# Performance work log

Hardware: AMD Instinct MI355X
Metric: run time of the kernel (lower is better)

The kernel has to match this reference:

```python
import jax, jax.numpy as jnp
import numpy as np

N_SPOT = 30000
N_USER = 30000
E = 600000
SPLIT = 5
ATT_IN = 512
HEADS = 4
PER = ATT_IN // HEADS  # 128
HID = 256
N_LAYERS = 3


def _glorot(key, shape):
    fan_in, fan_out = shape[-2], shape[-1]
    lim = (6.0 / (fan_in + fan_out)) ** 0.5
    return jax.random.uniform(key, shape, jnp.float32, -lim, lim)


def setup_inputs() -> dict:
    key = jax.random.key(0)
    ks = jax.random.split(key, 16)
    return {
        "x_spot": jax.random.normal(ks[0], (N_SPOT, SPLIT * ATT_IN), jnp.float32),
        "x_user": jax.random.normal(ks[1], (N_USER, 512), jnp.float32),
        "edge_us": jax.random.randint(ks[2], (2, E), 0, N_USER),  # user -> spot
        "edge_su": jax.random.randint(ks[3], (2, E), 0, N_SPOT),  # spot -> user
        "W_att": _glorot(ks[4], (HEADS, ATT_IN, PER)),
        "q_att": 1.414 * _glorot(ks[5], (HEADS, PER, 1)),
        "W0_us": _glorot(ks[6], (512, HID)),   # layer0 source weight, user->spot
        "W0_su": _glorot(ks[7], (512, HID)),   # layer0 source weight, spot->user
        "Wmid_us": _glorot(ks[8], (N_LAYERS - 1, HID, HID)),
        "Wmid_su": _glorot(ks[9], (N_LAYERS - 1, HID, HID)),
        "W_out_spot": _glorot(ks[10], (HID, 1)),
        "b_out_spot": jnp.zeros((1,), jnp.float32),
        "W_out_user": _glorot(ks[11], (HID, 1)),
        "b_out_user": jnp.zeros((1,), jnp.float32),
    }


def _edge_div(edge, n_src, n_dst):
    # sqrt(deg_src[e_src] * deg_dst[e_dst]) per edge (symmetric GCN normalization)
    deg_s = jnp.zeros((n_src,), jnp.float32).at[edge[0]].add(1.0)
    deg_t = jnp.zeros((n_dst,), jnp.float32).at[edge[1]].add(1.0)
    return jnp.sqrt(deg_s[edge[0]] * deg_t[edge[1]])


def _attention(x_spot, W_att, q_att):
    # x: [N, split, 512]; per head: project, softmax over split, weighted sum
    x = x_spot.reshape(-1, SPLIT, ATT_IN)
    xh = jnp.einsum('nsi,hio->hnso', x, W_att)                        # [H,N,S,PER]
    att = jax.nn.softmax(
        jax.nn.leaky_relu(jnp.einsum('hnso,hop->hnsp', xh, q_att), 0.2), axis=2)
    pooled = (xh * att).sum(axis=2)                                   # [H,N,PER]
    return jnp.moveaxis(pooled, 0, 1).reshape(x.shape[0], HEADS * PER)  # concat heads


def _conv(x_src, n_dst, edge, W_src, div):
    # per-edge-type linear on source nodes, gather, normalize, scatter-sum to targets
    msg = (x_src @ W_src)[edge[0]] / div[:, None]
    return jnp.zeros((n_dst, W_src.shape[1]), x_src.dtype).at[edge[1]].add(msg)


def reference(x_spot, x_user, edge_us, edge_su, W_att, q_att,
              W0_us, W0_su, Wmid_us, Wmid_su,
              W_out_spot, b_out_spot, W_out_user, b_out_user):
    div_us = _edge_div(edge_us, N_USER, N_SPOT)
    div_su = _edge_div(edge_su, N_SPOT, N_USER)

    xs = _attention(x_spot, W_att, q_att)  # spot features -> 512-d
    xu = x_user

    Ws_us = [W0_us] + [Wmid_us[i] for i in range(N_LAYERS - 1)]
    Ws_su = [W0_su] + [Wmid_su[i] for i in range(N_LAYERS - 1)]

    acc_s, acc_u = [], []
    for l in range(N_LAYERS):
        # div[node_type] == 1 here (one edge type per target); relu applied twice in
        # the original (post-div relu + ReLU flag) which is idempotent.
        new_s = jax.nn.relu(_conv(xu, N_SPOT, edge_us, Ws_us[l], div_us))
        new_u = jax.nn.relu(_conv(xs, N_USER, edge_su, Ws_su[l], div_su))
        xs, xu = new_s, new_u
        acc_s.append(xs)
        acc_u.append(xu)

    out_s = xs @ W_out_spot + b_out_spot
    out_u = xu @ W_out_user + b_out_user
    x_mean_s = jnp.mean(jnp.stack(acc_s, axis=0), axis=0)
    x_mean_u = jnp.mean(jnp.stack(acc_u, axis=0), axis=0)
    return (x_mean_s, x_mean_u, out_s, out_u)
```

## Files before the change

kernel.cpp:

```cpp
#include <hip/hip_runtime.h>
#include <hip/hip_bf16.h>

#define NN 30000
#define ATT_IN 512
#define HID 256

__global__ __launch_bounds__(256) void k_count_deg(
    const int* __restrict__ us, const int* __restrict__ su, int E,
    int* __restrict__ d_us_s, int* __restrict__ d_us_d,
    int* __restrict__ d_su_s, int* __restrict__ d_su_d) {
  int e = blockIdx.x * 256 + threadIdx.x;
  if (e < E) {
    atomicAdd(&d_us_s[us[e]], 1);
    atomicAdd(&d_us_d[us[E + e]], 1);
    atomicAdd(&d_su_s[su[e]], 1);
    atomicAdd(&d_su_d[su[E + e]], 1);
  }
}

__global__ __launch_bounds__(1024) void k_scan(
    const int* __restrict__ deg, int* __restrict__ rp, int n) {
  __shared__ int sums[1024];
  int t = threadIdx.x;
  int chunk = (n + 1023) / 1024;
  int lo = t * chunk, hi = lo + chunk;
  if (hi > n) hi = n;
  if (lo > n) lo = n;
  int s = 0;
  for (int i = lo; i < hi; ++i) s += deg[i];
  sums[t] = s;
  __syncthreads();
  for (int off = 1; off < 1024; off <<= 1) {
    int v = (t >= off) ? sums[t - off] : 0;
    __syncthreads();
    sums[t] += v;
    __syncthreads();
  }
  int run = sums[t] - s;
  for (int i = lo; i < hi; ++i) { rp[i] = run; run += deg[i]; }
  if (t == 1023) rp[n] = sums[1023];
}

__global__ __launch_bounds__(256) void k_fill_csr(
    const int* __restrict__ src, const int* __restrict__ dst,
    const int* __restrict__ deg_s, const int* __restrict__ deg_d,
    const int* __restrict__ rp, int* __restrict__ fill,
    int* __restrict__ col, float* __restrict__ wv, int E) {
  int e = blockIdx.x * 256 + threadIdx.x;
  if (e < E) {
    int s = src[e], d = dst[e];
    int pos = rp[d] + atomicAdd(&fill[d], 1);
    col[pos] = s;
    wv[pos] = 1.0f / sqrtf((float)deg_s[s] * (float)deg_d[d]);
  }
}

__global__ __launch_bounds__(256) void k_wq(
    const float* __restrict__ W_att, const float* __restrict__ q_att,
    float* __restrict__ wq) {
  int g = blockIdx.x * 256 + threadIdx.x;
  if (g < 4 * ATT_IN) {
    int h = g >> 9, i = g & 511;
    const float* w = W_att + (size_t)h * ATT_IN * 128 + (size_t)i * 128;
    const float* q = q_att + h * 128;
    float s = 0.f;
    for (int p = 0; p < 128; ++p) s += w[p] * q[p];
    wq[g] = s;
  }
}

__global__ __launch_bounds__(256) void k_att(
    const float* __restrict__ x_spot, const float* __restrict__ wq,
    float* __restrict__ att) {
  int wave = threadIdx.x >> 6, lane = threadIdx.x & 63;
  int n = blockIdx.x * 4 + wave;
  float wreg[4][8];
  for (int h = 0; h < 4; ++h) {
    const float4* p = (const float4*)(wq + h * ATT_IN + lane * 8);
    float4 a = p[0], b = p[1];
    wreg[h][0] = a.x; wreg[h][1] = a.y; wreg[h][2] = a.z; wreg[h][3] = a.w;
    wreg[h][4] = b.x; wreg[h][5] = b.y; wreg[h][6] = b.z; wreg[h][7] = b.w;
  }
  float part[5][4];
  const float* xrow = x_spot + (size_t)n * (5 * ATT_IN);
  for (int s = 0; s < 5; ++s) {
    const float4* p = (const float4*)(xrow + s * ATT_IN + lane * 8);
    float4 a = p[0], b = p[1];
    float xv[8] = {a.x, a.y, a.z, a.w, b.x, b.y, b.z, b.w};
    for (int h = 0; h < 4; ++h) {
      float acc = 0.f;
      for (int i = 0; i < 8; ++i) acc += xv[i] * wreg[h][i];
      part[s][h] = acc;
    }
  }
  for (int off = 32; off; off >>= 1)
    for (int s = 0; s < 5; ++s)
      for (int h = 0; h < 4; ++h)
        part[s][h] += __shfl_xor(part[s][h], off);
  if (lane < 20) {
    int h = lane / 5, s = lane % 5;
    float l[5];
    for (int s2 = 0; s2 < 5; ++s2) {
      float v = part[s2][h];
      l[s2] = v > 0.f ? v : 0.2f * v;
    }
    float m = l[0];
    for (int s2 = 1; s2 < 5; ++s2) m = fmaxf(m, l[s2]);
    float sum = 0.f;
    for (int s2 = 0; s2 < 5; ++s2) sum += expf(l[s2] - m);
    att[(size_t)n * 20 + h * 5 + s] = expf(l[s] - m) / sum;
  }
}

__global__ __launch_bounds__(256) void k_pooled(
    const float* __restrict__ x_spot, const float* __restrict__ W_att,
    const float* __restrict__ att, float* __restrict__ xs0) {
  __shared__ float As[16][68];
  __shared__ float Bs[16][132];
  int h = blockIdx.y;
  int mb = blockIdx.x * 64;
  int t = threadIdx.x;
  int ty = t >> 4, tx = t & 15;
  int ka = t & 15, ma0 = (t >> 4) * 4;
  int kb = t >> 5, nb0 = (t & 31) * 4;
  float a5[4][5];
  for (int i = 0; i < 4; ++i) {
    int n = mb + ma0 + i;
    for (int s = 0; s < 5; ++s)
      a5[i][s] = (n < NN) ? att[(size_t)n * 20 + h * 5 + s] : 0.f;
  }
  const float* Wh = W_att + (size_t)h * ATT_IN * 128;
  float acc[4][8];
  for (int i = 0; i < 4; ++i)
    for (int j = 0; j < 8; ++j) acc[i][j] = 0.f;

  for (int k0 = 0; k0 < ATT_IN; k0 += 16) {
    for (int i = 0; i < 4; ++i) {
      int n = mb + ma0 + i;
      float v = 0.f;
      if (n < NN) {
        const float* xr = x_spot + (size_t)n * (5 * ATT_IN) + k0 + ka;
        v = a5[i][0] * xr[0] + a5[i][1] * xr[512] + a5[i][2] * xr[1024]
          + a5[i][3] * xr[1536] + a5[i][4] * xr[2048];
      }
      As[ka][ma0 + i] = v;
    }
    for (int kk = kb; kk < 16; kk += 8) {
      const float4 bv = *(const float4*)&Wh[(size_t)(k0 + kk) * 128 + nb0];
      *(float4*)&Bs[kk][nb0] = bv;
    }
    __syncthreads();
    for (int k = 0; k < 16; ++k) {
      float4 av = *(const float4*)&As[k][ty * 4];
      float4 b0 = *(const float4*)&Bs[k][tx * 8];
      float4 b1 = *(const float4*)&Bs[k][tx * 8 + 4];
      float a[4] = {av.x, av.y, av.z, av.w};
      float b[8] = {b0.x, b0.y, b0.z, b0.w, b1.x, b1.y, b1.z, b1.w};
      for (int i = 0; i < 4; ++i)
        for (int j = 0; j < 8; ++j) acc[i][j] += a[i] * b[j];
    }
    __syncthreads();
  }
  for (int i = 0; i < 4; ++i) {
    int n = mb + ty * 4 + i;
    if (n < NN) {
      float4 o0 = {acc[i][0], acc[i][1], acc[i][2], acc[i][3]};
      float4 o1 = {acc[i][4], acc[i][5], acc[i][6], acc[i][7]};
      float* dst = xs0 + (size_t)n * ATT_IN + h * 128 + tx * 8;
      *(float4*)dst = o0;
      *(float4*)(dst + 4) = o1;
    }
  }
}

__global__ __launch_bounds__(256) void k_gemm(
    const float* __restrict__ A, const float* __restrict__ B,
    float* __restrict__ C, int M, int N, int K) {
  __shared__ float As[16][132];
  __shared__ float Bs[16][68];
  int mb = blockIdx.x * 128;
  int nb = blockIdx.y * 64;
  int t = threadIdx.x;
  int ty = t >> 4, tx = t & 15;
  int ka = t & 15, ma0 = (t >> 4) * 8;
  int kb = t >> 4, nb0 = (t & 15) * 4;
  float acc[8][4];
  for (int i = 0; i < 8; ++i)
    for (int j = 0; j < 4; ++j) acc[i][j] = 0.f;

  for (int k0 = 0; k0 < K; k0 += 16) {
    for (int i = 0; i < 8; ++i) {
      int m = mb + ma0 + i;
      As[ka][ma0 + i] = (m < M) ? A[(size_t)m * K + k0 + ka] : 0.f;
    }
    {
      const float4 bv = *(const float4*)&B[(size_t)(k0 + kb) * N + nb + nb0];
      *(float4*)&Bs[kb][nb0] = bv;
    }
    __syncthreads();
    for (int k = 0; k < 16; ++k) {
      float4 a0 = *(const float4*)&As[k][ty * 8];
      float4 a1 = *(const float4*)&As[k][ty * 8 + 4];
      float4 bv = *(const float4*)&Bs[k][tx * 4];
      float a[8] = {a0.x, a0.y, a0.z, a0.w, a1.x, a1.y, a1.z, a1.w};
      float b[4] = {bv.x, bv.y, bv.z, bv.w};
      for (int i = 0; i < 8; ++i)
        for (int j = 0; j < 4; ++j) acc[i][j] += a[i] * b[j];
    }
    __syncthreads();
  }
  for (int i = 0; i < 8; ++i) {
    int m = mb + ty * 8 + i;
    if (m < M) {
      float4 o = {acc[i][0], acc[i][1], acc[i][2], acc[i][3]};
      *(float4*)&C[(size_t)m * N + nb + tx * 4] = o;
    }
  }
}

__global__ __launch_bounds__(256) void k_spmm(
    const int* __restrict__ rp, const int* __restrict__ col,
    const float* __restrict__ wv, const float* __restrict__ tin,
    float* __restrict__ xout, float* __restrict__ meanout,
    const float* __restrict__ Wout, const float* __restrict__ bout,
    float* __restrict__ headout, int mode) {
  int wave = threadIdx.x >> 6, lane = threadIdx.x & 63;
  int n = blockIdx.x * 4 + wave;
  if (n >= NN) return;
  int j0 = rp[n], j1 = rp[n + 1];
  float ax = 0.f, ay = 0.f, az = 0.f, aw = 0.f;
  for (int j = j0; j < j1; ++j) {
    int src = col[j];
    float w = wv[j];
    const float4 v = *(const float4*)&tin[(size_t)src * HID + lane * 4];
    ax += w * v.x; ay += w * v.y; az += w * v.z; aw += w * v.w;
  }
  float4 val = {fmaxf(ax, 0.f), fmaxf(ay, 0.f), fmaxf(az, 0.f), fmaxf(aw, 0.f)};
  *(float4*)&xout[(size_t)n * HID + lane * 4] = val;
  float4* mp = (float4*)&meanout[(size_t)n * HID + lane * 4];
  if (mode == 0) {
    *mp = val;
  } else {
    float4 pm = *mp;
    pm.x += val.x; pm.y += val.y; pm.z += val.z; pm.w += val.w;
    if (mode == 2) {
      const float third = 1.f / 3.f;
      pm.x *= third; pm.y *= third; pm.z *= third; pm.w *= third;
    }
    *mp = pm;
  }
  if (mode == 2) {
    const float4 w4 = *(const float4*)&Wout[lane * 4];
    float d = val.x * w4.x + val.y * w4.y + val.z * w4.z + val.w * w4.w;
    for (int off = 32; off; off >>= 1) d += __shfl_xor(d, off);
    if (lane == 0) headout[n] = d + bout[0];
  }
}

extern "C" void kernel_launch(void* const* d_in, const int* in_sizes, int n_in,
                              void* d_out, int out_size, void* d_ws, size_t ws_size,
                              hipStream_t stream) {
  const float* x_spot  = (const float*)d_in[0];
  const float* x_user  = (const float*)d_in[1];
  const int*   edge_us = (const int*)d_in[2];
  const int*   edge_su = (const int*)d_in[3];
  const float* W_att   = (const float*)d_in[4];
  const float* q_att   = (const float*)d_in[5];
  const float* W0_us   = (const float*)d_in[6];
  const float* W0_su   = (const float*)d_in[7];
  const float* Wmid_us = (const float*)d_in[8];
  const float* Wmid_su = (const float*)d_in[9];
  const float* W_out_s = (const float*)d_in[10];
  const float* b_out_s = (const float*)d_in[11];
  const float* W_out_u = (const float*)d_in[12];
  const float* b_out_u = (const float*)d_in[13];

  const int E = in_sizes[2] / 2;

  float* out_mean_s = (float*)d_out;
  float* out_mean_u = out_mean_s + (size_t)NN * HID;
  float* out_s      = out_mean_u + (size_t)NN * HID;
  float* out_u      = out_s + NN;

  int*   wsI = (int*)d_ws;
  float* wsF = (float*)d_ws;
  int* deg_us_s = wsI + 0;
  int* deg_us_d = wsI + 30000;
  int* deg_su_s = wsI + 60000;
  int* deg_su_d = wsI + 90000;
  int* fill_s   = wsI + 120000;
  int* fill_u   = wsI + 150000;
  int* rp_s     = wsI + 180000;
  int* rp_u     = wsI + 210016;
  int* col_s    = wsI + 240032;
  int* col_u    = wsI + 840032;
  float* wv_s   = wsF + 1440032;
  float* wv_u   = wsF + 2040032;
  float* wq     = wsF + 2640032;
  float* att    = wsF + 2642080;
  float* xs0    = wsF + 3242080;
  float* xs     = wsF + 3242080;
  float* xu     = wsF + 10922080;
  float* t_u    = wsF + 18602080;
  float* t_s    = wsF + 26282080;

  const int EB = (E + 255) / 256;

  hipMemsetAsync(d_ws, 0, 180000 * sizeof(int), stream);

  k_count_deg<<<EB, 256, 0, stream>>>(edge_us, edge_su, E,
                                      deg_us_s, deg_us_d, deg_su_s, deg_su_d);
  k_scan<<<1, 1024, 0, stream>>>(deg_us_d, rp_s, NN);
  k_scan<<<1, 1024, 0, stream>>>(deg_su_d, rp_u, NN);
  k_fill_csr<<<EB, 256, 0, stream>>>(edge_us, edge_us + E, deg_us_s, deg_us_d,
                                     rp_s, fill_s, col_s, wv_s, E);
  k_fill_csr<<<EB, 256, 0, stream>>>(edge_su, edge_su + E, deg_su_s, deg_su_d,
                                     rp_u, fill_u, col_u, wv_u, E);

  k_wq<<<8, 256, 0, stream>>>(W_att, q_att, wq);
  k_att<<<NN / 4, 256, 0, stream>>>(x_spot, wq, att);
  k_pooled<<<dim3((NN + 63) / 64, 4), 256, 0, stream>>>(x_spot, W_att, att, xs0);

  const int MB = (NN + 127) / 128;

  k_gemm<<<dim3(MB, 4), 256, 0, stream>>>(x_user, W0_us, t_u, NN, HID, 512);
  k_gemm<<<dim3(MB, 4), 256, 0, stream>>>(xs0,    W0_su, t_s, NN, HID, 512);
  k_spmm<<<NN / 4, 256, 0, stream>>>(rp_s, col_s, wv_s, t_u, xs, out_mean_s,
                                     nullptr, nullptr, nullptr, 0);
  k_spmm<<<NN / 4, 256, 0, stream>>>(rp_u, col_u, wv_u, t_s, xu, out_mean_u,
                                     nullptr, nullptr, nullptr, 0);
  k_gemm<<<dim3(MB, 4), 256, 0, stream>>>(xu, Wmid_us,           t_u, NN, HID, HID);
  k_gemm<<<dim3(MB, 4), 256, 0, stream>>>(xs, Wmid_su,           t_s, NN, HID, HID);
  k_spmm<<<NN / 4, 256, 0, stream>>>(rp_s, col_s, wv_s, t_u, xs, out_mean_s,
                                     nullptr, nullptr, nullptr, 1);
  k_spmm<<<NN / 4, 256, 0, stream>>>(rp_u, col_u, wv_u, t_s, xu, out_mean_u,
                                     nullptr, nullptr, nullptr, 1);
  k_gemm<<<dim3(MB, 4), 256, 0, stream>>>(xu, Wmid_us + 256 * 256, t_u, NN, HID, HID);
  k_gemm<<<dim3(MB, 4), 256, 0, stream>>>(xs, Wmid_su + 256 * 256, t_s, NN, HID, HID);
  k_spmm<<<NN / 4, 256, 0, stream>>>(rp_s, col_s, wv_s, t_u, xs, out_mean_s,
                                     W_out_s, b_out_s, out_s, 2);
  k_spmm<<<NN / 4, 256, 0, stream>>>(rp_u, col_u, wv_u, t_s, xu, out_mean_u,
                                     W_out_u, b_out_u, out_u, 2);
}
```

Measured before the change: 2.279 ms.

## Fuse attention heads in pooled GEMM, widen GEMM tiles, unroll SpMM gather

The pooled attention kernel now handles all four heads in one block of 32 nodes, so the attention-weighted reduction of x_spot over the five splits is read once per node instead of once per head. That cuts the dominant global traffic on the 30000x2560 input. The generic GEMM moves to 128x128 tiles with 8x8 per-thread accumulators and padded shared-memory layouts to avoid bank conflicts, which raises register pressure. The SpMM gather loop is unrolled by two so two row loads are in flight at once.

```diff
diff --git a/kernel.cpp b/kernel.cpp
--- a/kernel.cpp
+++ b/kernel.cpp
@@ -4,6 +4,8 @@
 #define NN 30000
 #define ATT_IN 512
 #define HID 256
+
+#define GP(c) ((c) + 4 * ((c) >> 5))
 
 __global__ __launch_bounds__(256) void k_count_deg(
     const int* __restrict__ us, const int* __restrict__ su, int E,
@@ -112,108 +114,166 @@
   }
 }
 
-__global__ __launch_bounds__(256) void k_pooled(
+#define PLANEA 584
+#define PLANEB 2248
+__global__ __launch_bounds__(256) void k_pooled2(
     const float* __restrict__ x_spot, const float* __restrict__ W_att,
     const float* __restrict__ att, float* __restrict__ xs0) {
-  __shared__ float As[16][68];
-  __shared__ float Bs[16][132];
-  int h = blockIdx.y;
-  int mb = blockIdx.x * 64;
+  __shared__ float As[4 * PLANEA];
+  __shared__ float Bs[4 * PLANEB];
+  __shared__ float att_s[32][20];
   int t = threadIdx.x;
-  int ty = t >> 4, tx = t & 15;
-  int ka = t & 15, ma0 = (t >> 4) * 4;
-  int kb = t >> 5, nb0 = (t & 31) * 4;
-  float a5[4][5];
-  for (int i = 0; i < 4; ++i) {
-    int n = mb + ma0 + i;
-    for (int s = 0; s < 5; ++s)
-      a5[i][s] = (n < NN) ? att[(size_t)n * 20 + h * 5 + s] : 0.f;
-  }
-  const float* Wh = W_att + (size_t)h * ATT_IN * 128;
-  float acc[4][8];
-  for (int i = 0; i < 4; ++i)
+  int mb = blockIdx.x * 32;
+
+  if (t < 160) {
+    int m = t / 5, r4 = (t % 5) * 4;
+    int n = mb + m;
+    float4 v = make_float4(0.f, 0.f, 0.f, 0.f);
+    if (n < NN) v = *(const float4*)&att[(size_t)n * 20 + r4];
+    *(float4*)&att_s[m][r4] = v;
+  }
+  __syncthreads();
+
+  int fk = t & 15;
+  int fm = t >> 4;
+  float a5a[4][5], a5b[4][5];
+  #pragma unroll
+  for (int h = 0; h < 4; ++h)
+    #pragma unroll
+    for (int s = 0; s < 5; ++s) {
+      a5a[h][s] = att_s[fm][h * 5 + s];
+      a5b[h][s] = att_s[fm + 16][h * 5 + s];
+    }
+  int n_a = mb + fm, n_b = mb + fm + 16;
+  bool va = n_a < NN, vb = n_b < NN;
+  const float* xa = x_spot + (size_t)n_a * (5 * ATT_IN);
+  const float* xb = x_spot + (size_t)n_b * (5 * ATT_IN);
+
+  int wv_ = t >> 6;
+  int h  = (t & 63) >> 4;
+  int c0 = (t & 15) * 8;
+  int p0 = GP(c0);
+  int m0 = wv_ * 8;
+
+  float acc[8][8];
+  #pragma unroll
+  for (int i = 0; i < 8; ++i)
+    #pragma unroll
     for (int j = 0; j < 8; ++j) acc[i][j] = 0.f;
 
   for (int k0 = 0; k0 < ATT_IN; k0 += 16) {
-    for (int i = 0; i < 4; ++i) {
-      int n = mb + ma0 + i;
-      float v = 0.f;
-      if (n < NN) {
-        const float* xr = x_spot + (size_t)n * (5 * ATT_IN) + k0 + ka;
-        v = a5[i][0] * xr[0] + a5[i][1] * xr[512] + a5[i][2] * xr[1024]
-          + a5[i][3] * xr[1536] + a5[i][4] * xr[2048];
-      }
-      As[ka][ma0 + i] = v;
-    }
-    for (int kk = kb; kk < 16; kk += 8) {
-      const float4 bv = *(const float4*)&Wh[(size_t)(k0 + kk) * 128 + nb0];
-      *(float4*)&Bs[kk][nb0] = bv;
-    }
-    __syncthreads();
+    float xva[5], xvb[5];
+    #pragma unroll
+    for (int s = 0; s < 5; ++s) {
+      xva[s] = va ? xa[s * ATT_IN + k0 + fk] : 0.f;
+      xvb[s] = vb ? xb[s * ATT_IN + k0 + fk] : 0.f;
+    }
+    #pragma unroll
+    for (int hh = 0; hh < 4; ++hh) {
+      float sa = a5a[hh][0] * xva[0] + a5a[hh][1] * xva[1] + a5a[hh][2] * xva[2]
+               + a5a[hh][3] * xva[3] + a5a[hh][4] * xva[4];
+      float sb = a5b[hh][0] * xvb[0] + a5b[hh][1] * xvb[1] + a5b[hh][2] * xvb[2]
+               + a5b[hh][3] * xvb[3] + a5b[hh][4] * xvb[4];
+      As[hh * PLANEA + fk * 36 + fm]      = sa;
+      As[hh * PLANEA + fk * 36 + fm + 16] = sb;
+    }
+    #pragma unroll
+    for (int r = 0; r < 8; ++r) {
+      int flat = r * 256 + t;
+      int bh = flat >> 9, rem = flat & 511;
+      int bk = rem >> 5, bc = (rem & 31) * 4;
+      float4 w = *(const float4*)&W_att[(size_t)bh * ATT_IN * 128
+                                        + (size_t)(k0 + bk) * 128 + bc];
+      *(float4*)&Bs[bh * PLANEB + bk * 140 + GP(bc)] = w;
+    }
+    __syncthreads();
+    #pragma unroll
     for (int k = 0; k < 16; ++k) {
-      float4 av = *(const float4*)&As[k][ty * 4];
-      float4 b0 = *(const float4*)&Bs[k][tx * 8];
-      float4 b1 = *(const float4*)&Bs[k][tx * 8 + 4];
-      float a[4] = {av.x, av.y, av.z, av.w};
+      float4 a0 = *(const float4*)&As[h * PLANEA + k * 36 + m0];
+      float4 a1 = *(const float4*)&As[h * PLANEA + k * 36 + m0 + 4];
+      float4 b0 = *(const float4*)&Bs[h * PLANEB + k * 140 + p0];
+      float4 b1 = *(const float4*)&Bs[h * PLANEB + k * 140 + p0 + 4];
+      float a[8] = {a0.x, a0.y, a0.z, a0.w, a1.x, a1.y, a1.z, a1.w};
       float b[8] = {b0.x, b0.y, b0.z, b0.w, b1.x, b1.y, b1.z, b1.w};
-      for (int i = 0; i < 4; ++i)
+      #pragma unroll
+      for (int i = 0; i < 8; ++i)
+        #pragma unroll
         for (int j = 0; j < 8; ++j) acc[i][j] += a[i] * b[j];
     }
     __syncthreads();
   }
-  for (int i = 0; i < 4; ++i) {
-    int n = mb + ty * 4 + i;
+  #pragma unroll
+  for (int i = 0; i < 8; ++i) {
+    int n = mb + m0 + i;
     if (n < NN) {
       float4 o0 = {acc[i][0], acc[i][1], acc[i][2], acc[i][3]};
       float4 o1 = {acc[i][4], acc[i][5], acc[i][6], acc[i][7]};
-      float* dst = xs0 + (size_t)n * ATT_IN + h * 128 + tx * 8;
+      float* dst = xs0 + (size_t)n * ATT_IN + h * 128 + c0;
       *(float4*)dst = o0;
       *(float4*)(dst + 4) = o1;
     }
   }
 }
 
-__global__ __launch_bounds__(256) void k_gemm(
+__global__ __launch_bounds__(256) void k_gemm2(
     const float* __restrict__ A, const float* __restrict__ B,
     float* __restrict__ C, int M, int N, int K) {
-  __shared__ float As[16][132];
-  __shared__ float Bs[16][68];
+  __shared__ float As[16 * 140];
+  __shared__ float Bs[16 * 140];
   int mb = blockIdx.x * 128;
-  int nb = blockIdx.y * 64;
+  int nb = blockIdx.y * 128;
   int t = threadIdx.x;
   int ty = t >> 4, tx = t & 15;
   int ka = t & 15, ma0 = (t >> 4) * 8;
-  int kb = t >> 4, nb0 = (t & 15) * 4;
-  float acc[8][4];
+  int kb = t >> 4, nb0 = (t & 15) * 8;
+  int m0 = ty * 8, c0 = tx * 8;
+  int pm0 = GP(m0), pc0 = GP(c0);
+  int pa = ka * 140 + GP(ma0);
+  int pb = kb * 140 + GP(nb0);
+
+  float acc[8][8];
+  #pragma unroll
   for (int i = 0; i < 8; ++i)
-    for (int j = 0; j < 4; ++j) acc[i][j] = 0.f;
+    #pragma unroll
+    for (int j = 0; j < 8; ++j) acc[i][j] = 0.f;
 
   for (int k0 = 0; k0 < K; k0 += 16) {
+    #pragma unroll
     for (int i = 0; i < 8; ++i) {
       int m = mb + ma0 + i;
-      As[ka][ma0 + i] = (m < M) ? A[(size_t)m * K + k0 + ka] : 0.f;
+      As[pa + i] = (m < M) ? A[(size_t)m * K + k0 + ka] : 0.f;
     }
     {
-      const float4 bv = *(const float4*)&B[(size_t)(k0 + kb) * N + nb + nb0];
-      *(float4*)&Bs[kb][nb0] = bv;
-    }
-    __syncthreads();
+      float4 b0 = *(const float4*)&B[(size_t)(k0 + kb) * N + nb + nb0];
+      float4 b1 = *(const float4*)&B[(size_t)(k0 + kb) * N + nb + nb0 + 4];
+      *(float4*)&Bs[pb] = b0;
+      *(float4*)&Bs[pb + 4] = b1;
+    }
+    __syncthreads();
+    #pragma unroll
     for (int k = 0; k < 16; ++k) {
-      float4 a0 = *(const float4*)&As[k][ty * 8];
-      float4 a1 = *(const float4*)&As[k][ty * 8 + 4];
-      float4 bv = *(const float4*)&Bs[k][tx * 4];
+      float4 a0 = *(const float4*)&As[k * 140 + pm0];
+      float4 a1 = *(const float4*)&As[k * 140 + pm0 + 4];
+      float4 b0 = *(const float4*)&Bs[k * 140 + pc0];
+      float4 b1 = *(const float4*)&Bs[k * 140 + pc0 + 4];
       float a[8] = {a0.x, a0.y, a0.z, a0.w, a1.x, a1.y, a1.z, a1.w};
-      float b[4] = {bv.x, bv.y, bv.z, bv.w};
+      float b[8] = {b0.x, b0.y, b0.z, b0.w, b1.x, b1.y, b1.z, b1.w};
+      #pragma unroll
       for (int i = 0; i < 8; ++i)
-        for (int j = 0; j < 4; ++j) acc[i][j] += a[i] * b[j];
-    }
-    __syncthreads();
-  }
+        #pragma unroll
+        for (int j = 0; j < 8; ++j) acc[i][j] += a[i] * b[j];
+    }
+    __syncthreads();
+  }
+  #pragma unroll
   for (int i = 0; i < 8; ++i) {
-    int m = mb + ty * 8 + i;
+    int m = mb + m0 + i;
     if (m < M) {
-      float4 o = {acc[i][0], acc[i][1], acc[i][2], acc[i][3]};
-      *(float4*)&C[(size_t)m * N + nb + tx * 4] = o;
+      float4 o0 = {acc[i][0], acc[i][1], acc[i][2], acc[i][3]};
+      float4 o1 = {acc[i][4], acc[i][5], acc[i][6], acc[i][7]};
+      float* dst = C + (size_t)m * N + nb + c0;
+      *(float4*)dst = o0;
+      *(float4*)(dst + 4) = o1;
     }
   }
 }
@@ -229,11 +289,22 @@
   if (n >= NN) return;
   int j0 = rp[n], j1 = rp[n + 1];
   float ax = 0.f, ay = 0.f, az = 0.f, aw = 0.f;
-  for (int j = j0; j < j1; ++j) {
-    int src = col[j];
-    float w = wv[j];
-    const float4 v = *(const float4*)&tin[(size_t)src * HID + lane * 4];
-    ax += w * v.x; ay += w * v.y; az += w * v.z; aw += w * v.w;
+  int j = j0;
+  for (; j + 1 < j1; j += 2) {
+    int s0 = col[j], s1 = col[j + 1];
+    float w0 = wv[j], w1 = wv[j + 1];
+    const float4 v0 = *(const float4*)&tin[(size_t)s0 * HID + lane * 4];
+    const float4 v1 = *(const float4*)&tin[(size_t)s1 * HID + lane * 4];
+    ax += w0 * v0.x + w1 * v1.x;
+    ay += w0 * v0.y + w1 * v1.y;
+    az += w0 * v0.z + w1 * v1.z;
+    aw += w0 * v0.w + w1 * v1.w;
+  }
+  if (j < j1) {
+    int s0 = col[j];
+    float w0 = wv[j];
+    const float4 v0 = *(const float4*)&tin[(size_t)s0 * HID + lane * 4];
+    ax += w0 * v0.x; ay += w0 * v0.y; az += w0 * v0.z; aw += w0 * v0.w;
   }
   float4 val = {fmaxf(ax, 0.f), fmaxf(ay, 0.f), fmaxf(az, 0.f), fmaxf(aw, 0.f)};
   *(float4*)&xout[(size_t)n * HID + lane * 4] = val;
@@ -319,24 +390,24 @@
 
   k_wq<<<8, 256, 0, stream>>>(W_att, q_att, wq);
   k_att<<<NN / 4, 256, 0, stream>>>(x_spot, wq, att);
-  k_pooled<<<dim3((NN + 63) / 64, 4), 256, 0, stream>>>(x_spot, W_att, att, xs0);
+  k_pooled2<<<(NN + 31) / 32, 256, 0, stream>>>(x_spot, W_att, att, xs0);
 
   const int MB = (NN + 127) / 128;
 
-  k_gemm<<<dim3(MB, 4), 256, 0, stream>>>(x_user, W0_us, t_u, NN, HID, 512);
-  k_gemm<<<dim3(MB, 4), 256, 0, stream>>>(xs0,    W0_su, t_s, NN, HID, 512);
+  k_gemm2<<<dim3(MB, 2), 256, 0, stream>>>(x_user, W0_us, t_u, NN, HID, 512);
+  k_gemm2<<<dim3(MB, 2), 256, 0, stream>>>(xs0,    W0_su, t_s, NN, HID, 512);
   k_spmm<<<NN / 4, 256, 0, stream>>>(rp_s, col_s, wv_s, t_u, xs, out_mean_s,
                                      nullptr, nullptr, nullptr, 0);
   k_spmm<<<NN / 4, 256, 0, stream>>>(rp_u, col_u, wv_u, t_s, xu, out_mean_u,
                                      nullptr, nullptr, nullptr, 0);
-  k_gemm<<<dim3(MB, 4), 256, 0, stream>>>(xu, Wmid_us,           t_u, NN, HID, HID);
-  k_gemm<<<dim3(MB, 4), 256, 0, stream>>>(xs, Wmid_su,           t_s, NN, HID, HID);
+  k_gemm2<<<dim3(MB, 2), 256, 0, stream>>>(xu, Wmid_us,           t_u, NN, HID, HID);
+  k_gemm2<<<dim3(MB, 2), 256, 0, stream>>>(xs, Wmid_su,           t_s, NN, HID, HID);
   k_spmm<<<NN / 4, 256, 0, stream>>>(rp_s, col_s, wv_s, t_u, xs, out_mean_s,
                                      nullptr, nullptr, nullptr, 1);
   k_spmm<<<NN / 4, 256, 0, stream>>>(rp_u, col_u, wv_u, t_s, xu, out_mean_u,
                                      nullptr, nullptr, nullptr, 1);
-  k_gemm<<<dim3(MB, 4), 256, 0, stream>>>(xu, Wmid_us + 256 * 256, t_u, NN, HID, HID);
-  k_gemm<<<dim3(MB, 4), 256, 0, stream>>>(xs, Wmid_su + 256 * 256, t_s, NN, HID, HID);
+  k_gemm2<<<dim3(MB, 2), 256, 0, stream>>>(xu, Wmid_us + 256 * 256, t_u, NN, HID, HID);
+  k_gemm2<<<dim3(MB, 2), 256, 0, stream>>>(xs, Wmid_su + 256 * 256, t_s, NN, HID, HID);
   k_spmm<<<NN / 4, 256, 0, stream>>>(rp_s, col_s, wv_s, t_u, xs, out_mean_s,
                                      W_out_s, b_out_s, out_s, 2);
   k_spmm<<<NN / 4, 256, 0, stream>>>(rp_u, col_u, wv_u, t_s, xu, out_mean_u,
```

Measured after the change: 2.534 ms. 11.2% more time.
